# Optimization experiments

Hardware: AMD Instinct MI355X
Metric: run time of the kernel (lower is better)

Reference implementation:

```python
import jax, jax.numpy as jnp
import numpy as np

B, L, LATENT, HID, NTOK = 65536, 8, 256, 128, 5


def setup_inputs() -> dict:
    key = jax.random.key(0)
    ks = jax.random.split(key, 8)
    s = 0.05  # small init scale for stable GRU dynamics
    return {
        "latent_context": jax.random.normal(ks[0], (B, LATENT), jnp.float32),
        "target_sequence": jax.random.randint(ks[1], (B, L), 0, NTOK),
        "emb_table": jax.random.normal(ks[2], (NTOK + 1, HID), jnp.float32) * s,
        "W_ih": jax.random.normal(ks[3], (3 * LATENT, HID), jnp.float32) * s,
        "W_hh": jax.random.normal(ks[4], (3 * LATENT, LATENT), jnp.float32) * s,
        "b_ih": jnp.zeros((3 * LATENT,), jnp.float32),
        "b_hh": jnp.zeros((3 * LATENT,), jnp.float32),
        "W_out": jax.random.normal(ks[5], (NTOK, LATENT), jnp.float32) * s,
        "b_out": jnp.zeros((NTOK,), jnp.float32),
    }


def reference(latent_context, target_sequence, emb_table, W_ih, W_hh, b_ih, b_hh, W_out, b_out):
    b = latent_context.shape[0]
    start_idx = emb_table.shape[0] - 1  # start token index = num_tokens
    # Teacher forcing: input token at step 0 is <start>, then target[:, :-1]
    tokens = jnp.concatenate(
        [jnp.full((b, 1), start_idx, dtype=target_sequence.dtype), target_sequence[:, :-1]],
        axis=1,
    )  # (B, L)
    emb = emb_table[tokens]  # (B, L, HID) embedding gather, done once

    def gru_step(h, x):
        # x: (B, HID), h: (B, LATENT). PyTorch GRU cell math.
        gi = x @ W_ih.T + b_ih          # (B, 3*LATENT)
        gh = h @ W_hh.T + b_hh          # (B, 3*LATENT)
        i_r, i_z, i_n = jnp.split(gi, 3, axis=-1)
        h_r, h_z, h_n = jnp.split(gh, 3, axis=-1)
        r = jax.nn.sigmoid(i_r + h_r)
        z = jax.nn.sigmoid(i_z + h_z)
        n = jnp.tanh(i_n + r * h_n)
        h_new = (1.0 - z) * n + z * h
        step_logits = h_new @ W_out.T + b_out  # (B, NTOK)
        return h_new, step_logits

    _, logits = jax.lax.scan(gru_step, latent_context, jnp.swapaxes(emb, 0, 1))
    return jnp.swapaxes(logits, 0, 1)  # (B, L, NTOK)
```

## Files before the change

kernel.cpp:

```cpp
#include <hip/hip_runtime.h>
#include <hip/hip_bf16.h>


typedef __attribute__((ext_vector_type(8)))  __bf16 bf16x8;
typedef __attribute__((ext_vector_type(4)))  __bf16 bf16x4;
typedef __attribute__((ext_vector_type(4)))  float  f32x4;

#define LOG2E_F     1.4426950408889634f
#define TWO_LOG2E_F 2.8853900817779268f

#if __has_builtin(__builtin_amdgcn_exp2f)
#define EXP2F(x) __builtin_amdgcn_exp2f(x)
#else
#define EXP2F(x) __expf((x) * 0.6931471805599453f)
#endif

__device__ __forceinline__ float sigm2(float a) {
    return __builtin_amdgcn_rcpf(1.f + EXP2F(-a));
}
__device__ __forceinline__ float tanh2(float a) {
    return __builtin_fmaf(2.f, __builtin_amdgcn_rcpf(1.f + EXP2F(-a)), -1.f);
}
__device__ __forceinline__ void lds_barrier() {
    __builtin_amdgcn_sched_barrier(0);
    asm volatile("s_waitcnt lgkmcnt(0)" ::: "memory");
    __builtin_amdgcn_s_barrier();
    __builtin_amdgcn_sched_barrier(0);
}

#define MFMA16(a, b, c) __builtin_amdgcn_mfma_f32_16x16x32_bf16((a), (b), (c), 0, 0, 0)

__global__ void k_gtable(const float* __restrict__ emb, const float* __restrict__ W_ih,
                         const float* __restrict__ b_ih, const float* __restrict__ b_hh,
                         float* __restrict__ G) {
    int tok = blockIdx.x;
    int j   = threadIdx.x;
    const float4* e4 = (const float4*)(emb + tok * 128);
    const float4* w4 = (const float4*)(W_ih + (size_t)j * 128);
    float s = 0.f;
#pragma unroll
    for (int k = 0; k < 32; ++k) {
        float4 a = e4[k], b = w4[k];
        s += a.x * b.x + a.y * b.y + a.z * b.z + a.w * b.w;
    }
    s += b_ih[j];
    if (j < 512) s = (s + b_hh[j]) * LOG2E_F;
    else         s = s * TWO_LOG2E_F;
    G[tok * 768 + j] = s;
}

__global__ void k_wfrag3(const float* __restrict__ Whh, const float* __restrict__ Gtab,
                         const float* __restrict__ b_hh, __bf16* __restrict__ Wg) {
    int u    = blockIdx.x * 256 + threadIdx.x;
    int lane = u & 63;
    int frag = u >> 6;
    int w    = frag / 28;
    int f    = frag - 28 * w;
    int col  = w * 16 + (lane & 15);
    int kq   = lane >> 4;
    bf16x8 v;
    if (f < 24) {
        int g = f >> 3, kc = f & 7;
        float scale = (g < 2) ? LOG2E_F : TWO_LOG2E_F;
        const float* src = Whh + (size_t)(g * 256 + col) * 256 + kc * 32 + kq * 8;
#pragma unroll
        for (int j = 0; j < 8; ++j) v[j] = (__bf16)(src[j] * scale);
    } else {
        int g = f - 24;
#pragma unroll
        for (int j = 0; j < 8; ++j) {
            int k = kq * 8 + j;
            float val = 0.f;
            if (k < 6) {
                val = (g == 0) ? Gtab[k * 768 + col]
                    : (g == 1) ? Gtab[k * 768 + 256 + col]
                    : (g == 2) ? b_hh[512 + col] * TWO_LOG2E_F
                               : Gtab[k * 768 + 512 + col];
            }
            v[j] = (__bf16)val;
        }
    }
    *(bf16x8*)(Wg + (size_t)u * 8) = v;
}

__global__ __launch_bounds__(1024) void k_main(
    const float* __restrict__ latent, const int* __restrict__ tgt,
    const __bf16* __restrict__ Wg, const float* __restrict__ Wout,
    const float* __restrict__ bout, float* __restrict__ out) {

    __shared__ __bf16 h_lds[2][4][8][64][8];
    __shared__ __bf16 onehot_lds[8][4][64][8];
    __shared__ __bf16 woutf_lds[8][64][8];
    __shared__ float  logit_lds[64 * 40];

    const int tid  = threadIdx.x;
    const int lane = tid & 63;
    const int w    = tid >> 6;
    const int q    = lane >> 4;
    const int n16  = lane & 15;
    const int row0 = blockIdx.x * 64;

    const __bf16* wbase = Wg + ((size_t)(w * 28) * 64 + lane) * 8;

    const int kc_h  = w >> 1;
    const int slotl = n16 + 16 * ((2 * w + (q >> 1)) & 3);
    const int joff  = 4 * (q & 1);

    if (tid < 512) {
        int kc = tid >> 6, ln = tid & 63, m = ln & 15, kq2 = ln >> 4;
        bf16x8 v;
#pragma unroll
        for (int j = 0; j < 8; ++j)
            v[j] = (m < 5) ? (__bf16)Wout[m * 256 + kc * 32 + kq2 * 8 + j] : (__bf16)0.f;
        *(bf16x8*)&woutf_lds[kc][ln][0] = v;
    }
    for (int s = tid; s < 2048; s += 1024) {
        int t = s >> 8, nt = (s >> 6) & 3, ln = s & 63;
        int nn = ln & 15, kq2 = ln >> 4;
        int tok = (t == 0) ? 5 : tgt[(size_t)(row0 + nt * 16 + nn) * 8 + t - 1];
        bf16x8 v;
#pragma unroll
        for (int j = 0; j < 8; ++j) v[j] = (__bf16)((kq2 * 8 + j == tok) ? 1.f : 0.f);
        *(bf16x8*)&onehot_lds[t][nt][ln][0] = v;
    }
#pragma unroll
    for (int nt = 0; nt < 4; ++nt) {
        float4 hv = *(const float4*)(latent + (size_t)(row0 + nt * 16 + n16) * 256 + 16 * w + 4 * q);
        bf16x4 hb;
        hb[0] = (__bf16)hv.x; hb[1] = (__bf16)hv.y;
        hb[2] = (__bf16)hv.z; hb[3] = (__bf16)hv.w;
        *(bf16x4*)&h_lds[0][nt][kc_h][slotl][joff] = hb;
    }
    const int lw = (w == 0) ? 0 : (w == 5) ? 1 : (w == 10) ? 2 : (w == 15) ? 3 : -1;
    const float bo0 = bout[0], bo1 = bout[1], bo2 = bout[2], bo3 = bout[3], bo4 = bout[4];
    const f32x4 z4 = {0.f, 0.f, 0.f, 0.f};
    __syncthreads();

    for (int t = 0; t < 8; ++t) {
        const int cur = t & 1, nxt = cur ^ 1;
        f32x4 acc[4][4];

        __builtin_amdgcn_s_setprio(1);
        {
            bf16x8 a0 = *(const bf16x8*)(wbase + (size_t)24 * 512);
            bf16x8 a1 = *(const bf16x8*)(wbase + (size_t)25 * 512);
            bf16x8 a2 = *(const bf16x8*)(wbase + (size_t)26 * 512);
            bf16x8 a3 = *(const bf16x8*)(wbase + (size_t)27 * 512);
#pragma unroll
            for (int nt = 0; nt < 4; ++nt) {
                bf16x8 oh = *(const bf16x8*)&onehot_lds[t][nt][lane][0];
                acc[0][nt] = MFMA16(a0, oh, z4);
                acc[1][nt] = MFMA16(a1, oh, z4);
                acc[2][nt] = MFMA16(a2, oh, z4);
                acc[3][nt] = MFMA16(a3, oh, z4);
            }
        }
#pragma unroll 2
        for (int kc = 0; kc < 8; ++kc) {
            bf16x8 a0 = *(const bf16x8*)(wbase + (size_t)kc * 512);
            bf16x8 a1 = *(const bf16x8*)(wbase + (size_t)(8 + kc) * 512);
            bf16x8 a2 = *(const bf16x8*)(wbase + (size_t)(16 + kc) * 512);
#pragma unroll
            for (int nt = 0; nt < 4; ++nt) {
                bf16x8 bb = *(const bf16x8*)&h_lds[cur][nt][kc][lane][0];
                acc[0][nt] = MFMA16(a0, bb, acc[0][nt]);
                acc[1][nt] = MFMA16(a1, bb, acc[1][nt]);
                acc[2][nt] = MFMA16(a2, bb, acc[2][nt]);
            }
        }

        if (lw >= 0 && t > 0) {
            f32x4 lacc = z4;
#pragma unroll
            for (int kc = 0; kc < 8; ++kc) {
                bf16x8 wf = *(const bf16x8*)&woutf_lds[kc][lane][0];
                bf16x8 bb = *(const bf16x8*)&h_lds[cur][lw][kc][lane][0];
                lacc = MFMA16(wf, bb, lacc);
            }
            float* dst = &logit_lds[(lw * 16 + n16) * 40 + (t - 1) * 5];
            if (q == 0) {
                dst[0] = lacc[0] + bo0; dst[1] = lacc[1] + bo1;
                dst[2] = lacc[2] + bo2; dst[3] = lacc[3] + bo3;
            } else if (q == 1) {
                dst[4] = lacc[0] + bo4;
            }
        }
        __builtin_amdgcn_s_setprio(0);

#pragma unroll
        for (int nt = 0; nt < 4; ++nt) {
            bf16x4 hold = *(const bf16x4*)&h_lds[cur][nt][kc_h][slotl][joff];
            bf16x4 hb;
#pragma unroll
            for (int i = 0; i < 4; ++i) {
                float rg = sigm2(acc[0][nt][i]);
                float zg = sigm2(acc[1][nt][i]);
                float ng = tanh2(__builtin_fmaf(rg, acc[2][nt][i], acc[3][nt][i]));
                float hv = ng + zg * ((float)hold[i] - ng);
                hb[i] = (__bf16)hv;
            }
            *(bf16x4*)&h_lds[nxt][nt][kc_h][slotl][joff] = hb;
        }
        lds_barrier();
    }

    if (lw >= 0) {
        f32x4 lacc = z4;
#pragma unroll
        for (int kc = 0; kc < 8; ++kc) {
            bf16x8 wf = *(const bf16x8*)&woutf_lds[kc][lane][0];
            bf16x8 bb = *(const bf16x8*)&h_lds[0][lw][kc][lane][0];
            lacc = MFMA16(wf, bb, lacc);
        }
        float* dst = &logit_lds[(lw * 16 + n16) * 40 + 7 * 5];
        if (q == 0) {
            dst[0] = lacc[0] + bo0; dst[1] = lacc[1] + bo1;
            dst[2] = lacc[2] + bo2; dst[3] = lacc[3] + bo3;
        } else if (q == 1) {
            dst[4] = lacc[0] + bo4;
        }
    }
    __syncthreads();
    for (int i = tid; i < 64 * 40; i += 1024)
        out[(size_t)row0 * 40 + i] = logit_lds[i];
}

extern "C" void kernel_launch(void* const* d_in, const int* in_sizes, int n_in,
                              void* d_out, int out_size, void* d_ws, size_t ws_size,
                              hipStream_t stream) {
    const float* latent = (const float*)d_in[0];
    const int*   tgt    = (const int*)d_in[1];
    const float* emb    = (const float*)d_in[2];
    const float* W_ih   = (const float*)d_in[3];
    const float* W_hh   = (const float*)d_in[4];
    const float* b_ih   = (const float*)d_in[5];
    const float* b_hh   = (const float*)d_in[6];
    const float* W_out  = (const float*)d_in[7];
    const float* b_out  = (const float*)d_in[8];
    float* out = (float*)d_out;

    float*  Gtab = (float*)d_ws;
    __bf16* Wg   = (__bf16*)((char*)d_ws + 18432);

    k_gtable<<<6, 768, 0, stream>>>(emb, W_ih, b_ih, b_hh, Gtab);
    k_wfrag3<<<112, 256, 0, stream>>>(W_hh, Gtab, b_hh, Wg);
    k_main<<<1024, 1024, 0, stream>>>(latent, tgt, Wg, W_out, b_out, out);
}
```

Measured before the change: 247.1 us.

## Halve batch tile to 32 rows with 8 waves each owning two column slices

The main kernel now runs 2048 blocks of 512 threads, each handling 32 batch rows instead of 64. Each wave covers two 16-column slices of the hidden state, so it loads twice the weight fragments but reuses each h fragment across both slices. Launch bounds request 4 blocks per CU and the kc loop is no longer unrolled. The aim is more independent blocks per CU to hide barrier and latency stalls between GRU steps, at the cost of more register pressure and twice the total weight-fragment reads from global memory.

```diff
diff --git a/kernel.cpp b/kernel.cpp
--- a/kernel.cpp
+++ b/kernel.cpp
@@ -54,9 +54,9 @@
     int u    = blockIdx.x * 256 + threadIdx.x;
     int lane = u & 63;
     int frag = u >> 6;
-    int w    = frag / 28;
-    int f    = frag - 28 * w;
-    int col  = w * 16 + (lane & 15);
+    int s    = frag / 28;
+    int f    = frag - 28 * s;
+    int col  = s * 16 + (lane & 15);
     int kq   = lane >> 4;
     bf16x8 v;
     if (f < 24) {
@@ -83,30 +83,31 @@
     *(bf16x8*)(Wg + (size_t)u * 8) = v;
 }
 
-__global__ __launch_bounds__(1024) void k_main(
+__global__ __launch_bounds__(512, 4) void k_main(
     const float* __restrict__ latent, const int* __restrict__ tgt,
     const __bf16* __restrict__ Wg, const float* __restrict__ Wout,
     const float* __restrict__ bout, float* __restrict__ out) {
 
-    __shared__ __bf16 h_lds[2][4][8][64][8];
-    __shared__ __bf16 onehot_lds[8][4][64][8];
+    __shared__ __bf16 h_lds[2][2][8][64][8];
+    __shared__ __bf16 onehot_lds[8][2][64][8];
     __shared__ __bf16 woutf_lds[8][64][8];
-    __shared__ float  logit_lds[64 * 40];
+    __shared__ float  logit_lds[32 * 40];
 
     const int tid  = threadIdx.x;
     const int lane = tid & 63;
     const int w    = tid >> 6;
     const int q    = lane >> 4;
     const int n16  = lane & 15;
-    const int row0 = blockIdx.x * 64;
-
-    const __bf16* wbase = Wg + ((size_t)(w * 28) * 64 + lane) * 8;
-
-    const int kc_h  = w >> 1;
-    const int slotl = n16 + 16 * ((2 * w + (q >> 1)) & 3);
+    const int row0 = blockIdx.x * 32;
+
+    const __bf16* wb0 = Wg + ((size_t)((2 * w + 0) * 28) * 64 + lane) * 8;
+    const __bf16* wb1 = Wg + ((size_t)((2 * w + 1) * 28) * 64 + lane) * 8;
+
+    const int slot0 = n16 + 16 * ((q >> 1) & 3);
+    const int slot1 = n16 + 16 * ((2 + (q >> 1)) & 3);
     const int joff  = 4 * (q & 1);
 
-    if (tid < 512) {
+    {
         int kc = tid >> 6, ln = tid & 63, m = ln & 15, kq2 = ln >> 4;
         bf16x8 v;
 #pragma unroll
@@ -114,8 +115,8 @@
             v[j] = (m < 5) ? (__bf16)Wout[m * 256 + kc * 32 + kq2 * 8 + j] : (__bf16)0.f;
         *(bf16x8*)&woutf_lds[kc][ln][0] = v;
     }
-    for (int s = tid; s < 2048; s += 1024) {
-        int t = s >> 8, nt = (s >> 6) & 3, ln = s & 63;
+    for (int s = tid; s < 1024; s += 512) {
+        int t = s >> 7, nt = (s >> 6) & 1, ln = s & 63;
         int nn = ln & 15, kq2 = ln >> 4;
         int tok = (t == 0) ? 5 : tgt[(size_t)(row0 + nt * 16 + nn) * 8 + t - 1];
         bf16x8 v;
@@ -124,49 +125,59 @@
         *(bf16x8*)&onehot_lds[t][nt][ln][0] = v;
     }
 #pragma unroll
-    for (int nt = 0; nt < 4; ++nt) {
-        float4 hv = *(const float4*)(latent + (size_t)(row0 + nt * 16 + n16) * 256 + 16 * w + 4 * q);
-        bf16x4 hb;
-        hb[0] = (__bf16)hv.x; hb[1] = (__bf16)hv.y;
-        hb[2] = (__bf16)hv.z; hb[3] = (__bf16)hv.w;
-        *(bf16x4*)&h_lds[0][nt][kc_h][slotl][joff] = hb;
-    }
-    const int lw = (w == 0) ? 0 : (w == 5) ? 1 : (w == 10) ? 2 : (w == 15) ? 3 : -1;
+    for (int nt = 0; nt < 2; ++nt) {
+        const float* hrow = latent + (size_t)(row0 + nt * 16 + n16) * 256;
+#pragma unroll
+        for (int sl = 0; sl < 2; ++sl) {
+            float4 hv = *(const float4*)(hrow + 32 * w + 16 * sl + 4 * q);
+            bf16x4 hb;
+            hb[0] = (__bf16)hv.x; hb[1] = (__bf16)hv.y;
+            hb[2] = (__bf16)hv.z; hb[3] = (__bf16)hv.w;
+            *(bf16x4*)&h_lds[0][nt][w][sl ? slot1 : slot0][joff] = hb;
+        }
+    }
+    const int lw = (w == 0) ? 0 : (w == 5) ? 1 : -1;
     const float bo0 = bout[0], bo1 = bout[1], bo2 = bout[2], bo3 = bout[3], bo4 = bout[4];
     const f32x4 z4 = {0.f, 0.f, 0.f, 0.f};
     __syncthreads();
 
     for (int t = 0; t < 8; ++t) {
         const int cur = t & 1, nxt = cur ^ 1;
-        f32x4 acc[4][4];
+        f32x4 acc[4][2][2];
 
         __builtin_amdgcn_s_setprio(1);
         {
-            bf16x8 a0 = *(const bf16x8*)(wbase + (size_t)24 * 512);
-            bf16x8 a1 = *(const bf16x8*)(wbase + (size_t)25 * 512);
-            bf16x8 a2 = *(const bf16x8*)(wbase + (size_t)26 * 512);
-            bf16x8 a3 = *(const bf16x8*)(wbase + (size_t)27 * 512);
-#pragma unroll
-            for (int nt = 0; nt < 4; ++nt) {
-                bf16x8 oh = *(const bf16x8*)&onehot_lds[t][nt][lane][0];
-                acc[0][nt] = MFMA16(a0, oh, z4);
-                acc[1][nt] = MFMA16(a1, oh, z4);
-                acc[2][nt] = MFMA16(a2, oh, z4);
-                acc[3][nt] = MFMA16(a3, oh, z4);
-            }
-        }
-#pragma unroll 2
+            bf16x8 oh0 = *(const bf16x8*)&onehot_lds[t][0][lane][0];
+            bf16x8 oh1 = *(const bf16x8*)&onehot_lds[t][1][lane][0];
+#pragma unroll
+            for (int sl = 0; sl < 2; ++sl) {
+                const __bf16* wb = sl ? wb1 : wb0;
+                bf16x8 a0 = *(const bf16x8*)(wb + (size_t)24 * 512);
+                bf16x8 a1 = *(const bf16x8*)(wb + (size_t)25 * 512);
+                bf16x8 a2 = *(const bf16x8*)(wb + (size_t)26 * 512);
+                bf16x8 a3 = *(const bf16x8*)(wb + (size_t)27 * 512);
+                acc[0][sl][0] = MFMA16(a0, oh0, z4); acc[0][sl][1] = MFMA16(a0, oh1, z4);
+                acc[1][sl][0] = MFMA16(a1, oh0, z4); acc[1][sl][1] = MFMA16(a1, oh1, z4);
+                acc[2][sl][0] = MFMA16(a2, oh0, z4); acc[2][sl][1] = MFMA16(a2, oh1, z4);
+                acc[3][sl][0] = MFMA16(a3, oh0, z4); acc[3][sl][1] = MFMA16(a3, oh1, z4);
+            }
+        }
+#pragma unroll 1
         for (int kc = 0; kc < 8; ++kc) {
-            bf16x8 a0 = *(const bf16x8*)(wbase + (size_t)kc * 512);
-            bf16x8 a1 = *(const bf16x8*)(wbase + (size_t)(8 + kc) * 512);
-            bf16x8 a2 = *(const bf16x8*)(wbase + (size_t)(16 + kc) * 512);
-#pragma unroll
-            for (int nt = 0; nt < 4; ++nt) {
-                bf16x8 bb = *(const bf16x8*)&h_lds[cur][nt][kc][lane][0];
-                acc[0][nt] = MFMA16(a0, bb, acc[0][nt]);
-                acc[1][nt] = MFMA16(a1, bb, acc[1][nt]);
-                acc[2][nt] = MFMA16(a2, bb, acc[2][nt]);
-            }
+            bf16x8 b0 = *(const bf16x8*)&h_lds[cur][0][kc][lane][0];
+            bf16x8 b1 = *(const bf16x8*)&h_lds[cur][1][kc][lane][0];
+            bf16x8 a00 = *(const bf16x8*)(wb0 + (size_t)kc * 512);
+            bf16x8 a01 = *(const bf16x8*)(wb0 + (size_t)(8 + kc) * 512);
+            bf16x8 a02 = *(const bf16x8*)(wb0 + (size_t)(16 + kc) * 512);
+            bf16x8 a10 = *(const bf16x8*)(wb1 + (size_t)kc * 512);
+            bf16x8 a11 = *(const bf16x8*)(wb1 + (size_t)(8 + kc) * 512);
+            bf16x8 a12 = *(const bf16x8*)(wb1 + (size_t)(16 + kc) * 512);
+            acc[0][0][0] = MFMA16(a00, b0, acc[0][0][0]); acc[0][0][1] = MFMA16(a00, b1, acc[0][0][1]);
+            acc[1][0][0] = MFMA16(a01, b0, acc[1][0][0]); acc[1][0][1] = MFMA16(a01, b1, acc[1][0][1]);
+            acc[2][0][0] = MFMA16(a02, b0, acc[2][0][0]); acc[2][0][1] = MFMA16(a02, b1, acc[2][0][1]);
+            acc[0][1][0] = MFMA16(a10, b0, acc[0][1][0]); acc[0][1][1] = MFMA16(a10, b1, acc[0][1][1]);
+            acc[1][1][0] = MFMA16(a11, b0, acc[1][1][0]); acc[1][1][1] = MFMA16(a11, b1, acc[1][1][1]);
+            acc[2][1][0] = MFMA16(a12, b0, acc[2][1][0]); acc[2][1][1] = MFMA16(a12, b1, acc[2][1][1]);
         }
 
         if (lw >= 0 && t > 0) {
@@ -188,18 +199,22 @@
         __builtin_amdgcn_s_setprio(0);
 
 #pragma unroll
-        for (int nt = 0; nt < 4; ++nt) {
-            bf16x4 hold = *(const bf16x4*)&h_lds[cur][nt][kc_h][slotl][joff];
-            bf16x4 hb;
-#pragma unroll
-            for (int i = 0; i < 4; ++i) {
-                float rg = sigm2(acc[0][nt][i]);
-                float zg = sigm2(acc[1][nt][i]);
-                float ng = tanh2(__builtin_fmaf(rg, acc[2][nt][i], acc[3][nt][i]));
-                float hv = ng + zg * ((float)hold[i] - ng);
-                hb[i] = (__bf16)hv;
-            }
-            *(bf16x4*)&h_lds[nxt][nt][kc_h][slotl][joff] = hb;
+        for (int nt = 0; nt < 2; ++nt) {
+#pragma unroll
+            for (int sl = 0; sl < 2; ++sl) {
+                const int slot = sl ? slot1 : slot0;
+                bf16x4 hold = *(const bf16x4*)&h_lds[cur][nt][w][slot][joff];
+                bf16x4 hb;
+#pragma unroll
+                for (int i = 0; i < 4; ++i) {
+                    float rg = sigm2(acc[0][sl][nt][i]);
+                    float zg = sigm2(acc[1][sl][nt][i]);
+                    float ng = tanh2(__builtin_fmaf(rg, acc[2][sl][nt][i], acc[3][sl][nt][i]));
+                    float hv = ng + zg * ((float)hold[i] - ng);
+                    hb[i] = (__bf16)hv;
+                }
+                *(bf16x4*)&h_lds[nxt][nt][w][slot][joff] = hb;
+            }
         }
         lds_barrier();
     }
@@ -221,7 +236,7 @@
         }
     }
     __syncthreads();
-    for (int i = tid; i < 64 * 40; i += 1024)
+    for (int i = tid; i < 32 * 40; i += 512)
         out[(size_t)row0 * 40 + i] = logit_lds[i];
 }
 
@@ -244,5 +259,5 @@
 
     k_gtable<<<6, 768, 0, stream>>>(emb, W_ih, b_ih, b_hh, Gtab);
     k_wfrag3<<<112, 256, 0, stream>>>(W_hh, Gtab, b_hh, Wg);
-    k_main<<<1024, 1024, 0, stream>>>(latent, tgt, Wg, W_out, b_out, out);
-}
+    k_main<<<2048, 512, 0, stream>>>(latent, tgt, Wg, W_out, b_out, out);
+}
```

After: 296.1 us. 19.9% more time.
